# Kernel optimization log

Hardware: AMD Instinct MI355X
Metric: run time of the kernel (lower is better)

The kernel has to match this reference:

```python
import jax, jax.numpy as jnp
import numpy as np

N = 100000   # num_nodes
D = 128      # input_dim
DO = 128     # output_dim
V = 3        # num_views/relations
E = 500000   # edges per view
C = 2        # num_classes
H = D // 2   # label-attention hidden
VH = DO // 2 # view-attention hidden
EPS = 1e-5


def setup_inputs() -> dict:
    key = jax.random.key(0)
    ks = jax.random.split(key, 20)
    s = 0.05
    def nrm(k, shape):
        return jax.random.normal(k, shape, dtype=jnp.float32) * s
    return {
        'features': jax.random.normal(ks[0], (N, D), dtype=jnp.float32),
        'edge_src': jax.random.randint(ks[1], (V, E), 0, N, dtype=jnp.int32),
        'edge_dst': jax.random.randint(ks[2], (V, E), 0, N, dtype=jnp.int32),
        'edge_w': jax.random.uniform(ks[3], (V, E), dtype=jnp.float32),
        'clsW': nrm(ks[4], (D, C)), 'clsb': jnp.zeros((C,), jnp.float32),
        'attW1': nrm(ks[5], (C, D, H)), 'attb1': jnp.zeros((C, H), jnp.float32),
        'attW2': nrm(ks[6], (C, H)), 'attb2': jnp.zeros((C,), jnp.float32),
        'att_bias': jnp.float32(0.1),
        'relW': nrm(ks[7], (V, D, DO)), 'relb': jnp.zeros((V, DO), jnp.float32),
        'gateW': nrm(ks[8], (V, DO, DO)), 'gateb': jnp.zeros((V, DO), jnp.float32),
        'view_pref': jax.random.normal(ks[9], (V, DO), dtype=jnp.float32),
        'vattW1': nrm(ks[10], (DO, VH)), 'vattb1': jnp.zeros((VH,), jnp.float32),
        'vattW2': nrm(ks[11], (VH,)), 'vattb2': jnp.float32(0.0),
        'selfW': nrm(ks[12], (D, DO)), 'selfb': jnp.zeros((DO,), jnp.float32),
        'featW': nrm(ks[13], (D, DO)), 'featb': jnp.zeros((DO,), jnp.float32),
        'fusW': nrm(ks[14], (2 * DO, DO)), 'fusb': jnp.zeros((DO,), jnp.float32),
        'ln_g': jnp.ones((DO,), jnp.float32), 'ln_b': jnp.zeros((DO,), jnp.float32),
    }


def reference(features, edge_src, edge_dst, edge_w,
              clsW, clsb, attW1, attb1, attW2, attb2, att_bias,
              relW, relb, gateW, gateb,
              view_pref, vattW1, vattb1, vattW2, vattb2,
              selfW, selfb, featW, featb, fusW, fusb, ln_g, ln_b):
    # --- LabelAwareAttention ---
    class_probs = jax.nn.softmax(features @ clsW + clsb, axis=-1)          # [N,C]
    h = jax.nn.relu(jnp.einsum('nd,cdh->cnh', features, attW1) + attb1[:, None, :])
    scores = jax.nn.sigmoid(jnp.einsum('cnh,ch->cn', h, attW2) + attb2[:, None])
    node_att = jnp.sum(scores.T * class_probs, axis=-1) + att_bias         # [N]

    # --- per-view RelationAggregator (num_relations=1 -> relation weight is 1) ---
    src_f = features[edge_src]                                             # [V,E,D]
    msg = (jnp.einsum('ved,vdo->veo', src_f, relW) + relb[:, None, :]) \
          * edge_w[..., None]                                              # [V,E,DO]
    agg = jax.vmap(lambda m, d: jax.ops.segment_sum(m, d, num_segments=N))(
        msg, edge_dst)                                                     # [V,N,DO]
    gate = jax.nn.sigmoid(jnp.einsum('vno,vop->vnp', agg, gateW) + gateb[:, None, :])
    view_out = gate * agg                                                  # [V,N,DO]

    # --- ViewLevelAttention ---
    vh = jax.nn.relu(jnp.einsum('vno,oh->vnh', view_out * view_pref[:, None, :], vattW1) + vattb1)
    vscores = jnp.einsum('vnh,h->vn', vh, vattW2) + vattb2                 # [V,N]
    vweights = jax.nn.softmax(vscores, axis=0)                             # softmax over views
    combined = jnp.sum(view_out * vweights[..., None], axis=0)             # [N,DO]

    # --- fusion + residual + layer norm (dropout=0, eval) ---
    self_out = features @ selfW + selfb
    transformed = features @ featW + featb
    weighted = combined * node_att[:, None]
    fused = jax.nn.relu(jnp.concatenate([self_out, weighted], axis=-1) @ fusW + fusb)
    out = fused + transformed
    mu = jnp.mean(out, axis=-1, keepdims=True)
    var = jnp.var(out, axis=-1, keepdims=True)
    out = (out - mu) / jnp.sqrt(var + EPS) * ln_g + ln_b
    return out, class_probs
```

## Files before the change

### kernel.cpp

```cpp
#include <hip/hip_runtime.h>
#include <hip/hip_bf16.h>

#define NN 100000
#define DD 128
#define VV 3
#define EE 500000
#define TOT (VV * NN)
#define NB ((TOT + 255) / 256)
#define RGB ((NN + 127) / 128)

typedef unsigned short u16;
typedef unsigned int u32;
typedef short s8v __attribute__((ext_vector_type(8)));
typedef float f4v __attribute__((ext_vector_type(4)));

__device__ __forceinline__ float bf2f(u16 u) {
    return __uint_as_float(((u32)u) << 16);
}
__device__ __forceinline__ u16 f2bf(float f) {
    u32 x = __float_as_uint(f);
    u32 r = (x + 0x7fffu + ((x >> 16) & 1u)) >> 16;
    return (u16)r;
}

__device__ __forceinline__ void atomAddBf16x2(u16* addr, float f0, float f1) {
#if __has_builtin(__builtin_amdgcn_global_atomic_fadd_v2bf16)
    typedef short v2s __attribute__((ext_vector_type(2)));
    typedef v2s __attribute__((address_space(1)))* v2s_gp;
    v2s v;
    v.x = (short)f2bf(f0);
    v.y = (short)f2bf(f1);
    __builtin_amdgcn_global_atomic_fadd_v2bf16((v2s_gp)(void*)addr, v);
#else
    u32* p = (u32*)addr;
    u32 old = *(volatile u32*)p;
    while (true) {
        float lo = bf2f((u16)(old & 0xffffu)) + f0;
        float hi = bf2f((u16)(old >> 16)) + f1;
        u32 nv = (u32)f2bf(lo) | ((u32)f2bf(hi) << 16);
        u32 prev = atomicCAS(p, old, nv);
        if (prev == old) break;
        old = prev;
    }
#endif
}

template<int XSTR, int WSTR>
__device__ __forceinline__ void gemm16(float acc[4][4], const float* Xs,
                                       const float* Ws, int n0, int o0, int kbase) {
    #pragma unroll 4
    for (int kk = 0; kk < 64; kk += 4) {
        float4 w0 = *reinterpret_cast<const float4*>(Ws + (kk + 0) * WSTR + o0);
        float4 w1 = *reinterpret_cast<const float4*>(Ws + (kk + 1) * WSTR + o0);
        float4 w2 = *reinterpret_cast<const float4*>(Ws + (kk + 2) * WSTR + o0);
        float4 w3 = *reinterpret_cast<const float4*>(Ws + (kk + 3) * WSTR + o0);
// ... 75 lines not shown
    size_t o = ((size_t)v * 128 + n) * 128 + k;
    size_t i = ((size_t)v * 128 + k) * 128 + n;
    relWb[o]  = f2bf(relW[i]);
    gateWb[o] = f2bf(gateW[i]);
}

__global__ __launch_bounds__(128) void wprep2_kernel(
        const float* __restrict__ Wsf, const float* __restrict__ featW,
        const float* __restrict__ fusW,
        u16* __restrict__ WsfB, u16* __restrict__ featWB, u16* __restrict__ fusWbB) {
    int k = threadIdx.x;
    int n = blockIdx.x;
    WsfB[n * 128 + k]   = f2bf(Wsf[k * 128 + n]);
    featWB[n * 128 + k] = f2bf(featW[k * 128 + n]);
    fusWbB[n * 128 + k] = f2bf(fusW[(size_t)(128 + k) * 128 + n]);
}

__global__ __launch_bounds__(128) void wprep3_kernel(
        const float* __restrict__ attW1, u16* __restrict__ attW1B) {
    int k = threadIdx.x;
    int o = blockIdx.x;
    int c = o >> 6, h = o & 63;
    attW1B[o * 128 + k] = f2bf(attW1[((size_t)c * 128 + k) * 64 + h]);
}

__global__ __launch_bounds__(128) void wprep4_kernel(
        const float* __restrict__ vattW1, const float* __restrict__ view_pref,
        u16* __restrict__ vattW1p) {
    int k = threadIdx.x;
    int h = blockIdx.x & 63;
    int v = blockIdx.x >> 6;
    vattW1p[((size_t)v * 64 + h) * 128 + k] =
        f2bf(view_pref[v * 128 + k] * vattW1[k * 64 + h]);
}

__global__ __launch_bounds__(256) void featconv_kernel(
        const float* __restrict__ feat, u16* __restrict__ featB) {
    int t = blockIdx.x * 256 + threadIdx.x;
    float4 q = *reinterpret_cast<const float4*>(feat + (size_t)t * 4);
    ushort4 r;
    r.x = f2bf(q.x); r.y = f2bf(q.y); r.z = f2bf(q.z); r.w = f2bf(q.w);
    *reinterpret_cast<ushort4*>(featB + (size_t)t * 4) = r;
}


__global__ __launch_bounds__(256) void count_kernel(
        const int* __restrict__ edst, int* __restrict__ C) {
    int t = blockIdx.x * 256 + threadIdx.x;
    if (t >= VV * EE) return;
    int v = t / EE;
    atomicAdd(&C[v * NN + edst[t]], 1);
}

__global__ __launch_bounds__(256) void scanA_kernel(
        const int* __restrict__ C, int* __restrict__ bs) {
    int b = blockIdx.x, t = threadIdx.x;
    int i = b * 256 + t;
    int v = (i < TOT) ? C[i] : 0;
    __shared__ int s[256];
    s[t] = v;
    __syncthreads();
    #pragma unroll
    for (int off = 128; off > 0; off >>= 1) {
        if (t < off) s[t] += s[t + off];
        __syncthreads();
    }
// ... 297 lines not shown
    __syncthreads();
    if (tid < 64) {
        int n = tid >> 1, cc = tid & 1;
        float l = 0.f;
        for (int k = 0; k < 128; k += 4) {
            float4 x = *reinterpret_cast<const float4*>(&Xs[n][k]);
            l += x.x * clsW[(k + 0) * 2 + cc];
            l += x.y * clsW[(k + 1) * 2 + cc];
            l += x.z * clsW[(k + 2) * 2 + cc];
            l += x.w * clsW[(k + 3) * 2 + cc];
        }
        Lsc[n * 2 + cc] = l + clsb[cc];
        float s = 0.f;
        for (int u = 0; u < 16; ++u) s += red[n * 33 + cc * 16 + u];
        s += attb2[cc];
        Ssc[n * 2 + cc] = 1.f / (1.f + expf(-s));
    }
    __syncthreads();
    if (tid < 32) {
        int n = tid;
        float l0 = Lsc[n * 2], l1 = Lsc[n * 2 + 1];
        float m = fmaxf(l0, l1);
        float e0 = expf(l0 - m), e1 = expf(l1 - m);
        float inv = 1.f / (e0 + e1);
        float p0 = e0 * inv, p1 = e1 * inv;
        float na = p0 * Ssc[n * 2] + p1 * Ssc[n * 2 + 1] + att_bias[0];
        int row = row0 + n;
        node_att[row] = na;
        probs_out[row * 2]     = p0;
        probs_out[row * 2 + 1] = p1;
    }
}

__global__ __launch_bounds__(256) void relgate_mfma_kernel(
        const u16* __restrict__ relWb, const float* __restrict__ relb,
        const u16* __restrict__ gateWb, const float* __restrict__ gateb,
        const u16* __restrict__ vattW1p, const float* __restrict__ vattb1,
        const float* __restrict__ vattW2, const float* __restrict__ vattb2,
        u16* __restrict__ aggB, const float* __restrict__ wsum,
        float* __restrict__ vscores) {
    __shared__ u16 Xs[128][136];
    __shared__ u16 Wt[128][72];
    int tid = threadIdx.x;
    int wv = tid >> 6, lane = tid & 63;
    int quad = lane >> 4, l15 = lane & 15;
    int v = blockIdx.y;
    int row0 = blockIdx.x * 128;
    const size_t vbase = (size_t)v * NN;

    #pragma unroll
    for (int rep = 0; rep < 8; ++rep) {
        int flat = rep * 256 + tid;
        int n = flat >> 4, c8 = flat & 15;
        int gr = row0 + n; if (gr >= NN) gr = NN - 1;
        uint4 q = *reinterpret_cast<const uint4*>(aggB + (vbase + gr) * DD + c8 * 8);
        *reinterpret_cast<uint4*>(&Xs[n][c8 * 8]) = q;
    }

    f4v acc1[2][8], acc2[2][8];
    #pragma unroll
    for (int rt = 0; rt < 2; ++rt)
        #pragma unroll
        for (int c = 0; c < 8; ++c) {
            acc1[rt][c] = f4v{0.f, 0.f, 0.f, 0.f};
            acc2[rt][c] = f4v{0.f, 0.f, 0.f, 0.f};
        }

    const u16* W1 = relWb + (size_t)v * DD * DD;
    const u16* W2 = gateWb + (size_t)v * DD * DD;

    #pragma unroll
    for (int h = 0; h < 2; ++h) {
        #pragma unroll
        for (int rep = 0; rep < 4; ++rep) {
            int flat = rep * 256 + tid;
            int n = flat >> 3, c8 = flat & 7;
            uint4 q = *reinterpret_cast<const uint4*>(W1 + (size_t)n * DD + h * 64 + c8 * 8);
            *reinterpret_cast<uint4*>(&Wt[n][c8 * 8]) = q;
        }
        __syncthreads();
        #pragma unroll
        for (int t = 0; t < 2; ++t) {
            int kl = t * 32 + quad * 8;
            s8v a0 = *reinterpret_cast<const s8v*>(&Xs[wv * 32 + l15][h * 64 + kl]);
            s8v a1 = *reinterpret_cast<const s8v*>(&Xs[wv * 32 + 16 + l15][h * 64 + kl]);
            #pragma unroll
            for (int c = 0; c < 8; ++c) {
                s8v b = *reinterpret_cast<const s8v*>(&Wt[c * 16 + l15][kl]);
                acc1[0][c] = __builtin_amdgcn_mfma_f32_16x16x32_bf16(a0, b, acc1[0][c], 0, 0, 0);
                acc1[1][c] = __builtin_amdgcn_mfma_f32_16x16x32_bf16(a1, b, acc1[1][c], 0, 0, 0);
            }
        }
        __syncthreads();
    }

    float wsn[2][4], rb[8];
    #pragma unroll
    for (int rt = 0; rt < 2; ++rt)
        #pragma unroll
        for (int r = 0; r < 4; ++r) {
            int gr = row0 + wv * 32 + rt * 16 + quad * 4 + r;
            wsn[rt][r] = wsum[vbase + (gr < NN ? gr : NN - 1)];
        }
    #pragma unroll
    for (int c = 0; c < 8; ++c) rb[c] = relb[v * DD + c * 16 + l15];
    #pragma unroll
    for (int rt = 0; rt < 2; ++rt)
        #pragma unroll
        for (int c = 0; c < 8; ++c)
            #pragma unroll
            for (int r = 0; r < 4; ++r)
                acc1[rt][c][r] += wsn[rt][r] * rb[c];

    #pragma unroll
    for (int rt = 0; rt < 2; ++rt)
        #pragma unroll
        for (int c = 0; c < 8; ++c)
            #pragma unroll
            for (int r = 0; r < 4; ++r)
                Xs[wv * 32 + rt * 16 + quad * 4 + r][c * 16 + l15] = f2bf(acc1[rt][c][r]);
    __syncthreads();

    #pragma unroll
    for (int h = 0; h < 2; ++h) {
        #pragma unroll
        for (int rep = 0; rep < 4; ++rep) {
            int flat = rep * 256 + tid;
            int n = flat >> 3, c8 = flat & 7;
            uint4 q = *reinterpret_cast<const uint4*>(W2 + (size_t)n * DD + h * 64 + c8 * 8);
            *reinterpret_cast<uint4*>(&Wt[n][c8 * 8]) = q;
        }
        __syncthreads();
        #pragma unroll
        for (int t = 0; t < 2; ++t) {
            int kl = t * 32 + quad * 8;
            s8v a0 = *reinterpret_cast<const s8v*>(&Xs[wv * 32 + l15][h * 64 + kl]);
            s8v a1 = *reinterpret_cast<const s8v*>(&Xs[wv * 32 + 16 + l15][h * 64 + kl]);
            #pragma unroll
            for (int c = 0; c < 8; ++c) {
                s8v b = *reinterpret_cast<const s8v*>(&Wt[c * 16 + l15][kl]);
                acc2[0][c] = __builtin_amdgcn_mfma_f32_16x16x32_bf16(a0, b, acc2[0][c], 0, 0, 0);
                acc2[1][c] = __builtin_amdgcn_mfma_f32_16x16x32_bf16(a1, b, acc2[1][c], 0, 0, 0);
            }
        }
        __syncthreads();
    }

    float gb[8];
    #pragma unroll
    for (int c = 0; c < 8; ++c) gb[c] = gateb[v * DD + c * 16 + l15];
    #pragma unroll
    for (int rt = 0; rt < 2; ++rt)
        #pragma unroll
        for (int c = 0; c < 8; ++c)
            #pragma unroll
            for (int r = 0; r < 4; ++r) {
                float g = 1.f / (1.f + expf(-(acc2[rt][c][r] + gb[c])));
                Xs[wv * 32 + rt * 16 + quad * 4 + r][c * 16 + l15] = f2bf(g * acc1[rt][c][r]);
            }

    {
        const u16* Wv = vattW1p + (size_t)v * 64 * DD;
        #pragma unroll
        for (int rep = 0; rep < 4; ++rep) {
            int flat = rep * 256 + tid;
            int n = flat >> 4, c8 = flat & 15;
            uint4 q = *reinterpret_cast<const uint4*>(Wv + (size_t)n * DD + c8 * 8);
            int half = c8 >> 3;
            *reinterpret_cast<uint4*>(&Wt[half * 64 + n][(c8 & 7) * 8]) = q;
        }
    }
    __syncthreads();

    #pragma unroll
    for (int rep = 0; rep < 8; ++rep) {
        int flat = rep * 256 + tid;
        int n = flat >> 4, c8 = flat & 15;
        int gr = row0 + n;
        if (gr < NN)
            *reinterpret_cast<uint4*>(aggB + (vbase + gr) * DD + c8 * 8) =
                *reinterpret_cast<const uint4*>(&Xs[n][c8 * 8]);
    }

    f4v acc3[2][4];
    #pragma unroll
    for (int rt = 0; rt < 2; ++rt)
        #pragma unroll
        for (int c = 0; c < 4; ++c)
            acc3[rt][c] = f4v{0.f, 0.f, 0.f, 0.f};
    #pragma unroll
    for (int h = 0; h < 2; ++h) {
        #pragma unroll
        for (int t = 0; t < 2; ++t) {
            int kl = t * 32 + quad * 8;
            s8v a0 = *reinterpret_cast<const s8v*>(&Xs[wv * 32 + l15][h * 64 + kl]);
            s8v a1 = *reinterpret_cast<const s8v*>(&Xs[wv * 32 + 16 + l15][h * 64 + kl]);
            #pragma unroll
            for (int c = 0; c < 4; ++c) {
                s8v b = *reinterpret_cast<const s8v*>(&Wt[h * 64 + c * 16 + l15][kl]);
                acc3[0][c] = __builtin_amdgcn_mfma_f32_16x16x32_bf16(a0, b, acc3[0][c], 0, 0, 0);
                acc3[1][c] = __builtin_amdgcn_mfma_f32_16x16x32_bf16(a1, b, acc3[1][c], 0, 0, 0);
            }
        }
    }
    float vb1[4], vw2[4];
    #pragma unroll
    for (int c = 0; c < 4; ++c) {
        int col = c * 16 + l15;
        vb1[c] = vattb1[col];
        vw2[c] = vattW2[col];
    }
    float vb2 = vattb2[0];
    #pragma unroll
    for (int rt = 0; rt < 2; ++rt)
        #pragma unroll
        for (int r = 0; r < 4; ++r) {
            float p = 0.f;
            #pragma unroll
            for (int c = 0; c < 4; ++c) {
                float hv = acc3[rt][c][r] + vb1[c];
                hv = hv > 0.f ? hv : 0.f;
                p += hv * vw2[c];
            }
            #pragma unroll
            for (int m = 1; m < 16; m <<= 1)
                p += __shfl_xor(p, m);
            int gr = row0 + wv * 32 + rt * 16 + quad * 4 + r;
            if (l15 == 0 && gr < NN)
                vscores[vbase + gr] = p + vb2;
        }
}

__global__ __launch_bounds__(256) void relgate_kernel(
        const float* __restrict__ relW, const float* __restrict__ relb,
        const float* __restrict__ gateW, const float* __restrict__ gateb,
        u16* __restrict__ aggB, const float* __restrict__ wsum) {
    __shared__ float Xs[32][128];
// ... 110 lines not shown
    #pragma unroll
    for (int i = 0; i < 4; ++i) red[(n0 + i) * 17 + to] = part[i];
    __syncthreads();
    if (tid < 32) {
        float s = 0.f;
        for (int u = 0; u < 16; ++u) s += red[tid * 17 + u];
        vscores[(size_t)v * NN + row0 + tid] = s + vattb2[0];
    }
}

__global__ __launch_bounds__(256) void combine_kernel(
        u16* __restrict__ aggB, const float* __restrict__ vscores,
        const float* __restrict__ node_att) {
    int t = blockIdx.x * 256 + threadIdx.x;
    int n = t >> 5, c4 = t & 31;
    float s0 = vscores[n], s1 = vscores[NN + n], s2 = vscores[2 * NN + n];
    float m = fmaxf(s0, fmaxf(s1, s2));
    float e0 = expf(s0 - m), e1 = expf(s1 - m), e2 = expf(s2 - m);
    float inv = 1.f / (e0 + e1 + e2);
    float w0 = e0 * inv, w1 = e1 * inv, w2 = e2 * inv;
    float na = node_att[n];
    size_t off = (size_t)n * DD + c4 * 4;
    ushort4 q0 = *reinterpret_cast<const ushort4*>(aggB + off);
    ushort4 q1 = *reinterpret_cast<const ushort4*>(aggB + (size_t)NN * DD + off);
    ushort4 q2 = *reinterpret_cast<const ushort4*>(aggB + 2 * (size_t)NN * DD + off);
    ushort4 r;
    r.x = f2bf((bf2f(q0.x) * w0 + bf2f(q1.x) * w1 + bf2f(q2.x) * w2) * na);
    r.y = f2bf((bf2f(q0.y) * w0 + bf2f(q1.y) * w1 + bf2f(q2.y) * w2) * na);
    r.z = f2bf((bf2f(q0.z) * w0 + bf2f(q1.z) * w1 + bf2f(q2.z) * w2) * na);
    r.w = f2bf((bf2f(q0.w) * w0 + bf2f(q1.w) * w1 + bf2f(q2.w) * w2) * na);
    *reinterpret_cast<ushort4*>(aggB + off) = r;
}

__global__ __launch_bounds__(256) void final_mfma_kernel(
        const u16* __restrict__ featB, const u16* __restrict__ aggB,
        const float* __restrict__ vsc, const float* __restrict__ natt,
        const u16* __restrict__ WsfB, const u16* __restrict__ featWB,
        const u16* __restrict__ fusWbB,
        const float* __restrict__ c1, const float* __restrict__ featb,
        const float* __restrict__ ln_g, const float* __restrict__ ln_b,
        float* __restrict__ outp) {
    __shared__ u16 Xs[128][136];
    __shared__ u16 Wt[128][72];
    __shared__ float rw[3][128];
    int tid = threadIdx.x;
    int wv = tid >> 6, lane = tid & 63;
    int quad = lane >> 4, l15 = lane & 15;
    int row0 = blockIdx.x * 128;

    #pragma unroll
    for (int rep = 0; rep < 8; ++rep) {
        int flat = rep * 256 + tid;
        int n = flat >> 4, c8 = flat & 15;
        int gr = row0 + n; if (gr >= NN) gr = NN - 1;
        uint4 q = *reinterpret_cast<const uint4*>(featB + (size_t)gr * DD + c8 * 8);
        *reinterpret_cast<uint4*>(&Xs[n][c8 * 8]) = q;
    }
    if (tid < 128) {
        int gr = row0 + tid; if (gr >= NN) gr = NN - 1;
        float s0 = vsc[gr], s1 = vsc[NN + gr], s2 = vsc[2 * NN + gr];
        float m = fmaxf(s0, fmaxf(s1, s2));
        float e0 = expf(s0 - m), e1 = expf(s1 - m), e2 = expf(s2 - m);
        float inv = 1.f / (e0 + e1 + e2);
        float na = natt[gr];
        rw[0][tid] = e0 * inv * na;
        rw[1][tid] = e1 * inv * na;
        rw[2][tid] = e2 * inv * na;
    }

    f4v acc1[2][8], acc2[2][8];
    #pragma unroll
    for (int rt = 0; rt < 2; ++rt)
        #pragma unroll
        for (int c = 0; c < 8; ++c) {
            acc1[rt][c] = f4v{0.f, 0.f, 0.f, 0.f};
            acc2[rt][c] = f4v{0.f, 0.f, 0.f, 0.f};
        }

    #pragma unroll
    for (int h = 0; h < 2; ++h) {
        #pragma unroll
        for (int rep = 0; rep < 4; ++rep) {
            int flat = rep * 256 + tid;
            int n = flat >> 3, c8 = flat & 7;
            uint4 q = *reinterpret_cast<const uint4*>(WsfB + (size_t)n * DD + h * 64 + c8 * 8);
            *reinterpret_cast<uint4*>(&Wt[n][c8 * 8]) = q;
        }
        __syncthreads();
        #pragma unroll
        for (int t = 0; t < 2; ++t) {
            int kl = t * 32 + quad * 8;
            s8v a0 = *reinterpret_cast<const s8v*>(&Xs[wv * 32 + l15][h * 64 + kl]);
            s8v a1 = *reinterpret_cast<const s8v*>(&Xs[wv * 32 + 16 + l15][h * 64 + kl]);
            #pragma unroll
            for (int c = 0; c < 8; ++c) {
                s8v b = *reinterpret_cast<const s8v*>(&Wt[c * 16 + l15][kl]);
                acc1[0][c] = __builtin_amdgcn_mfma_f32_16x16x32_bf16(a0, b, acc1[0][c], 0, 0, 0);
                acc1[1][c] = __builtin_amdgcn_mfma_f32_16x16x32_bf16(a1, b, acc1[1][c], 0, 0, 0);
            }
        }
        __syncthreads();
        #pragma unroll
        for (int rep = 0; rep < 4; ++rep) {
            int flat = rep * 256 + tid;
            int n = flat >> 3, c8 = flat & 7;
            uint4 q = *reinterpret_cast<const uint4*>(featWB + (size_t)n * DD + h * 64 + c8 * 8);
            *reinterpret_cast<uint4*>(&Wt[n][c8 * 8]) = q;
        }
        __syncthreads();
        #pragma unroll
        for (int t = 0; t < 2; ++t) {
            int kl = t * 32 + quad * 8;
            s8v a0 = *reinterpret_cast<const s8v*>(&Xs[wv * 32 + l15][h * 64 + kl]);
            s8v a1 = *reinterpret_cast<const s8v*>(&Xs[wv * 32 + 16 + l15][h * 64 + kl]);
            #pragma unroll
            for (int c = 0; c < 8; ++c) {
                s8v b = *reinterpret_cast<const s8v*>(&Wt[c * 16 + l15][kl]);
                acc2[0][c] = __builtin_amdgcn_mfma_f32_16x16x32_bf16(a0, b, acc2[0][c], 0, 0, 0);
                acc2[1][c] = __builtin_amdgcn_mfma_f32_16x16x32_bf16(a1, b, acc2[1][c], 0, 0, 0);
            }
        }
        __syncthreads();
    }

    #pragma unroll
    for (int rep = 0; rep < 8; ++rep) {
        int flat = rep * 256 + tid;
        int n = flat >> 4, c8 = flat & 15;
        int gr = row0 + n; if (gr >= NN) gr = NN - 1;
        size_t off = (size_t)gr * DD + c8 * 8;
        uint4 q0 = *reinterpret_cast<const uint4*>(aggB + off);
        uint4 q1 = *reinterpret_cast<const uint4*>(aggB + (size_t)NN * DD + off);
        uint4 q2 = *reinterpret_cast<const uint4*>(aggB + 2 * (size_t)NN * DD + off);
        float w0 = rw[0][n], w1 = rw[1][n], w2 = rw[2][n];
        u32 o[4];
        const u32* a = &q0.x; const u32* b = &q1.x; const u32* c = &q2.x;
        #pragma unroll
        for (int j = 0; j < 4; ++j) {
            float lo = bf2f((u16)(a[j] & 0xffffu)) * w0 + bf2f((u16)(b[j] & 0xffffu)) * w1
                     + bf2f((u16)(c[j] & 0xffffu)) * w2;
            float hi = bf2f((u16)(a[j] >> 16)) * w0 + bf2f((u16)(b[j] >> 16)) * w1
                     + bf2f((u16)(c[j] >> 16)) * w2;
            o[j] = (u32)f2bf(lo) | ((u32)f2bf(hi) << 16);
        }
        uint4 r; r.x = o[0]; r.y = o[1]; r.z = o[2]; r.w = o[3];
        *reinterpret_cast<uint4*>(&Xs[n][c8 * 8]) = r;
    }
    #pragma unroll
    for (int h = 0; h < 2; ++h) {
        #pragma unroll
        for (int rep = 0; rep < 4; ++rep) {
            int flat = rep * 256 + tid;
            int n = flat >> 3, c8 = flat & 7;
            uint4 q = *reinterpret_cast<const uint4*>(fusWbB + (size_t)n * DD + h * 64 + c8 * 8);
            *reinterpret_cast<uint4*>(&Wt[n][c8 * 8]) = q;
        }
        __syncthreads();
        #pragma unroll
        for (int t = 0; t < 2; ++t) {
            int kl = t * 32 + quad * 8;
            s8v a0 = *reinterpret_cast<const s8v*>(&Xs[wv * 32 + l15][h * 64 + kl]);
            s8v a1 = *reinterpret_cast<const s8v*>(&Xs[wv * 32 + 16 + l15][h * 64 + kl]);
            #pragma unroll
            for (int c = 0; c < 8; ++c) {
                s8v b = *reinterpret_cast<const s8v*>(&Wt[c * 16 + l15][kl]);
                acc1[0][c] = __builtin_amdgcn_mfma_f32_16x16x32_bf16(a0, b, acc1[0][c], 0, 0, 0);
                acc1[1][c] = __builtin_amdgcn_mfma_f32_16x16x32_bf16(a1, b, acc1[1][c], 0, 0, 0);
            }
        }
        __syncthreads();
    }

    float c1j[8], fbj[8], gj[8], bj[8];
    #pragma unroll
    for (int c = 0; c < 8; ++c) {
        int col = c * 16 + l15;
        c1j[c] = c1[col];
        fbj[c] = featb[col];
        gj[c]  = ln_g[col];
        bj[c]  = ln_b[col];
    }
    #pragma unroll
    for (int rt = 0; rt < 2; ++rt)
        #pragma unroll
        for (int c = 0; c < 8; ++c)
            #pragma unroll
            for (int r = 0; r < 4; ++r) {
                float f = acc1[rt][c][r] + c1j[c];
                f = f > 0.f ? f : 0.f;
                acc1[rt][c][r] = f + acc2[rt][c][r] + fbj[c];
            }
    #pragma unroll
    for (int rt = 0; rt < 2; ++rt)
        #pragma unroll
        for (int r = 0; r < 4; ++r) {
            float s = 0.f, q = 0.f;
            #pragma unroll
            for (int c = 0; c < 8; ++c) {
                float x = acc1[rt][c][r];
                s += x; q += x * x;
            }
            #pragma unroll
            for (int m = 1; m < 16; m <<= 1) {
// ... 115 lines not shown
    const float* attb2     = (const float*)d_in[9];
    const float* att_bias  = (const float*)d_in[10];
    const float* relW      = (const float*)d_in[11];
    const float* relb      = (const float*)d_in[12];
    const float* gateW     = (const float*)d_in[13];
    const float* gateb     = (const float*)d_in[14];
    const float* view_pref = (const float*)d_in[15];
    const float* vattW1    = (const float*)d_in[16];
    const float* vattb1    = (const float*)d_in[17];
    const float* vattW2    = (const float*)d_in[18];
    const float* vattb2    = (const float*)d_in[19];
    const float* selfW     = (const float*)d_in[20];
    const float* selfb     = (const float*)d_in[21];
    const float* featW     = (const float*)d_in[22];
    const float* featb     = (const float*)d_in[23];
    const float* fusW      = (const float*)d_in[24];
    const float* fusb      = (const float*)d_in[25];
    const float* ln_g      = (const float*)d_in[26];
    const float* ln_b      = (const float*)d_in[27];

    u16*   aggB = (u16*)d_ws;
    float* wsum = (float*)(aggB + (size_t)VV * NN * DD);
    float* natt = wsum + (size_t)VV * NN;
    float* vsc  = natt + NN;
    float* Wsf  = vsc + (size_t)VV * NN;
    float* c1   = Wsf + DD * DD;
    u16* relWb  = (u16*)(c1 + DD);
    u16* gateWb = relWb + (size_t)VV * DD * DD;
    u16* WsfB   = gateWb + (size_t)VV * DD * DD;
    u16* featWB = WsfB + DD * DD;
    u16* fusWbB = featWB + DD * DD;
    u16* attW1B = fusWbB + DD * DD;
    u16* vattW1p = attW1B + DD * DD;
    int*   C    = (int*)(vattW1p + (size_t)VV * 64 * DD);
    int*   bs   = C + (size_t)TOT;
    int2*  bsw  = (int2*)(bs + NB + 1);
    u16* featB  = (u16*)(bsw + (size_t)VV * EE);
    size_t needed = (size_t)((char*)(featB + (size_t)NN * DD) - (char*)d_ws);

    float* outp  = (float*)d_out;
    float* probs = outp + (size_t)NN * DD;

    prep_kernel<<<129, 128, 0, stream>>>(selfW, selfb, fusW, fusb, Wsf, c1);
    if (ws_size >= needed) {
        featconv_kernel<<<12500, 256, 0, stream>>>(feat, featB);
        wprep_kernel<<<384, 128, 0, stream>>>(relW, gateW, relWb, gateWb);
        wprep2_kernel<<<128, 128, 0, stream>>>(Wsf, featW, fusW, WsfB, featWB, fusWbB);
        wprep3_kernel<<<128, 128, 0, stream>>>(attW1, attW1B);
        wprep4_kernel<<<192, 128, 0, stream>>>(vattW1, view_pref, vattW1p);
        label_mfma_kernel<<<RGB, 256, 0, stream>>>(featB, attW1B, clsW, clsb, attb1,
                                                   attW2, attb2, att_bias, natt, probs);
        hipMemsetAsync(C, 0, (size_t)TOT * sizeof(int), stream);
        count_kernel<<<(VV * EE + 255) / 256, 256, 0, stream>>>(edst, C);
        scanA_kernel<<<NB, 256, 0, stream>>>(C, bs);
        scanB_kernel<<<1, 1024, 0, stream>>>(bs);
        scanC_kernel<<<NB, 256, 0, stream>>>(C, bs);
        fill_kernel<<<(VV * EE + 255) / 256, 256, 0, stream>>>(esrc, edst, ew, C, bsw);
        gather_kernel<<<(VV * NN) / 4, 256, 0, stream>>>(featB, C, bsw, aggB, wsum);
        relgate_mfma_kernel<<<dim3(RGB, 3), 256, 0, stream>>>(relWb, relb, gateWb, gateb,
                                                              vattW1p, vattb1, vattW2, vattb2,
                                                              aggB, wsum, vsc);
        final_mfma_kernel<<<RGB, 256, 0, stream>>>(featB, aggB, vsc, natt,
                                                   WsfB, featWB, fusWbB,
                                                   c1, featb, ln_g, ln_b, outp);
    } else {
        label_kernel<<<3125, 256, 0, stream>>>(feat, clsW, clsb, attW1, attb1, attW2, attb2,
                                               att_bias, natt, probs);
        hipMemsetAsync(d_ws, 0,
                       (size_t)VV * NN * DD * sizeof(u16) + (size_t)VV * NN * sizeof(float),
                       stream);
        scatter_kernel<<<187500, 256, 0, stream>>>(esrc, edst, ew, feat, aggB, wsum);
        relgate_kernel<<<dim3(3125, 3), 256, 0, stream>>>(relW, relb, gateW, gateb, aggB, wsum);
        vatt_kernel<<<dim3(3125, 3), 128, 0, stream>>>(aggB, view_pref, vattW1, vattb1,
                                                       vattW2, vattb2, vsc);
        combine_kernel<<<12500, 256, 0, stream>>>(aggB, vsc, natt);
        final_kernel<<<3125, 256, 0, stream>>>(feat, aggB, Wsf, c1, fusW, featW, featb,
                                               ln_g, ln_b, outp);
    }
}
```

Baseline: 677.1 us.

## Precompose relW·gateW so rel and gate GEMMs run in parallel from registers

Adds a prep kernel that precomputes the product of relW and gateW (plus relb times gateW), so the gate pre-activation comes straight from agg and no longer waits on the rel output. This lets both GEMMs share A fragments held in registers, with fewer LDS round-trips and barriers. Final_mfma likewise loads A fragments into registers once and stages full weight tiles, and the softmax and sigmoid now use exp2/rcp intrinsics. Occupancy hints are added as launch bounds. The trade-offs are higher register pressure and a small numerical difference, since the composed weight is rounded to bf16.

```diff
diff --git a/kernel.cpp b/kernel.cpp
--- a/kernel.cpp
+++ b/kernel.cpp
@@ -21,6 +21,24 @@
     u32 x = __float_as_uint(f);
     u32 r = (x + 0x7fffu + ((x >> 16) & 1u)) >> 16;
     return (u16)r;
+}
+
+__device__ __forceinline__ float fexp2(float x) {
+#if __has_builtin(__builtin_amdgcn_exp2f)
+    return __builtin_amdgcn_exp2f(x);
+#else
+    return exp2f(x);
+#endif
+}
+__device__ __forceinline__ float frcp(float x) {
+#if __has_builtin(__builtin_amdgcn_rcpf)
+    return __builtin_amdgcn_rcpf(x);
+#else
+    return 1.f / x;
+#endif
+}
+__device__ __forceinline__ float fsigmoid(float x) {
+    return frcp(1.f + fexp2(-1.4426950408889634f * x));
 }
 
 __device__ __forceinline__ void atomAddBf16x2(u16* addr, float f0, float f1) {
@@ -162,6 +180,28 @@
     int v = blockIdx.x >> 6;
     vattW1p[((size_t)v * 64 + h) * 128 + k] =
         f2bf(view_pref[v * 128 + k] * vattW1[k * 64 + h]);
+}
+
+__global__ __launch_bounds__(128) void wprep5_kernel(
+        const float* __restrict__ relW, const float* __restrict__ gateW,
+        const float* __restrict__ relb,
+        u16* __restrict__ W12b, float* __restrict__ rgb) {
+    int p = threadIdx.x;
+    int b = blockIdx.x;
+    int v = b / 129;
+    int d = b - v * 129;
+    const float* gW = gateW + (size_t)v * 128 * 128;
+    if (d < 128) {
+        const float* rW = relW + ((size_t)v * 128 + d) * 128;
+        float acc = 0.f;
+        for (int o = 0; o < 128; ++o) acc += rW[o] * gW[o * 128 + p];
+        W12b[((size_t)v * 128 + p) * 128 + d] = f2bf(acc);
+    } else {
+        const float* rb = relb + (size_t)v * 128;
+        float acc = 0.f;
+        for (int o = 0; o < 128; ++o) acc += rb[o] * gW[o * 128 + p];
+        rgb[v * 128 + p] = acc;
+    }
 }
 
 __global__ __launch_bounds__(256) void featconv_kernel(
@@ -525,14 +565,15 @@
     }
 }
 
-__global__ __launch_bounds__(256) void relgate_mfma_kernel(
+__global__ __launch_bounds__(256, 3) void relgate_mfma_kernel(
         const u16* __restrict__ relWb, const float* __restrict__ relb,
-        const u16* __restrict__ gateWb, const float* __restrict__ gateb,
+        const u16* __restrict__ W12b, const float* __restrict__ rgb,
+        const float* __restrict__ gateb,
         const u16* __restrict__ vattW1p, const float* __restrict__ vattb1,
         const float* __restrict__ vattW2, const float* __restrict__ vattb2,
         u16* __restrict__ aggB, const float* __restrict__ wsum,
         float* __restrict__ vscores) {
-    __shared__ u16 Xs[128][136];
+    __shared__ u16 Wf[128][136];
     __shared__ u16 Wt[128][72];
     int tid = threadIdx.x;
     int wv = tid >> 6, lane = tid & 63;
@@ -547,8 +588,38 @@
         int n = flat >> 4, c8 = flat & 15;
         int gr = row0 + n; if (gr >= NN) gr = NN - 1;
         uint4 q = *reinterpret_cast<const uint4*>(aggB + (vbase + gr) * DD + c8 * 8);
-        *reinterpret_cast<uint4*>(&Xs[n][c8 * 8]) = q;
-    }
+        *reinterpret_cast<uint4*>(&Wf[n][c8 * 8]) = q;
+    }
+    __syncthreads();
+
+    s8v af[2][2][2];
+    #pragma unroll
+    for (int h = 0; h < 2; ++h)
+        #pragma unroll
+        for (int t = 0; t < 2; ++t) {
+            int kl = h * 64 + t * 32 + quad * 8;
+            af[h][t][0] = *reinterpret_cast<const s8v*>(&Wf[wv * 32 + l15][kl]);
+            af[h][t][1] = *reinterpret_cast<const s8v*>(&Wf[wv * 32 + 16 + l15][kl]);
+        }
+    __syncthreads();
+
+    const u16* W1 = relWb + (size_t)v * DD * DD;
+    const u16* W2 = W12b + (size_t)v * DD * DD;
+    #pragma unroll
+    for (int rep = 0; rep < 8; ++rep) {
+        int flat = rep * 256 + tid;
+        int n = flat >> 4, c8 = flat & 15;
+        *reinterpret_cast<uint4*>(&Wf[n][c8 * 8]) =
+            *reinterpret_cast<const uint4*>(W1 + (size_t)n * DD + c8 * 8);
+    }
+    #pragma unroll
+    for (int rep = 0; rep < 4; ++rep) {
+        int flat = rep * 256 + tid;
+        int n = flat >> 3, c8 = flat & 7;
+        *reinterpret_cast<uint4*>(&Wt[n][c8 * 8]) =
+            *reinterpret_cast<const uint4*>(W2 + (size_t)n * DD + c8 * 8);
+    }
+    __syncthreads();
 
     f4v acc1[2][8], acc2[2][8];
     #pragma unroll
@@ -559,35 +630,50 @@
             acc2[rt][c] = f4v{0.f, 0.f, 0.f, 0.f};
         }
 
-    const u16* W1 = relWb + (size_t)v * DD * DD;
-    const u16* W2 = gateWb + (size_t)v * DD * DD;
-
-    #pragma unroll
-    for (int h = 0; h < 2; ++h) {
-        #pragma unroll
-        for (int rep = 0; rep < 4; ++rep) {
-            int flat = rep * 256 + tid;
-            int n = flat >> 3, c8 = flat & 7;
-            uint4 q = *reinterpret_cast<const uint4*>(W1 + (size_t)n * DD + h * 64 + c8 * 8);
-            *reinterpret_cast<uint4*>(&Wt[n][c8 * 8]) = q;
-        }
-        __syncthreads();
+    #pragma unroll
+    for (int h = 0; h < 2; ++h)
         #pragma unroll
         for (int t = 0; t < 2; ++t) {
-            int kl = t * 32 + quad * 8;
-            s8v a0 = *reinterpret_cast<const s8v*>(&Xs[wv * 32 + l15][h * 64 + kl]);
-            s8v a1 = *reinterpret_cast<const s8v*>(&Xs[wv * 32 + 16 + l15][h * 64 + kl]);
+            int kl = h * 64 + t * 32 + quad * 8;
             #pragma unroll
             for (int c = 0; c < 8; ++c) {
-                s8v b = *reinterpret_cast<const s8v*>(&Wt[c * 16 + l15][kl]);
-                acc1[0][c] = __builtin_amdgcn_mfma_f32_16x16x32_bf16(a0, b, acc1[0][c], 0, 0, 0);
-                acc1[1][c] = __builtin_amdgcn_mfma_f32_16x16x32_bf16(a1, b, acc1[1][c], 0, 0, 0);
-            }
-        }
-        __syncthreads();
-    }
-
-    float wsn[2][4], rb[8];
+                s8v b = *reinterpret_cast<const s8v*>(&Wf[c * 16 + l15][kl]);
+                acc1[0][c] = __builtin_amdgcn_mfma_f32_16x16x32_bf16(af[h][t][0], b, acc1[0][c], 0, 0, 0);
+                acc1[1][c] = __builtin_amdgcn_mfma_f32_16x16x32_bf16(af[h][t][1], b, acc1[1][c], 0, 0, 0);
+            }
+        }
+    #pragma unroll
+    for (int t = 0; t < 2; ++t) {
+        int kl = t * 32 + quad * 8;
+        #pragma unroll
+        for (int c = 0; c < 8; ++c) {
+            s8v b = *reinterpret_cast<const s8v*>(&Wt[c * 16 + l15][kl]);
+            acc2[0][c] = __builtin_amdgcn_mfma_f32_16x16x32_bf16(af[0][t][0], b, acc2[0][c], 0, 0, 0);
+            acc2[1][c] = __builtin_amdgcn_mfma_f32_16x16x32_bf16(af[0][t][1], b, acc2[1][c], 0, 0, 0);
+        }
+    }
+    __syncthreads();
+
+    #pragma unroll
+    for (int rep = 0; rep < 4; ++rep) {
+        int flat = rep * 256 + tid;
+        int n = flat >> 3, c8 = flat & 7;
+        *reinterpret_cast<uint4*>(&Wt[n][c8 * 8]) =
+            *reinterpret_cast<const uint4*>(W2 + (size_t)n * DD + 64 + c8 * 8);
+    }
+    __syncthreads();
+    #pragma unroll
+    for (int t = 0; t < 2; ++t) {
+        int kl = t * 32 + quad * 8;
+        #pragma unroll
+        for (int c = 0; c < 8; ++c) {
+            s8v b = *reinterpret_cast<const s8v*>(&Wt[c * 16 + l15][kl]);
+            acc2[0][c] = __builtin_amdgcn_mfma_f32_16x16x32_bf16(af[1][t][0], b, acc2[0][c], 0, 0, 0);
+            acc2[1][c] = __builtin_amdgcn_mfma_f32_16x16x32_bf16(af[1][t][1], b, acc2[1][c], 0, 0, 0);
+        }
+    }
+
+    float wsn[2][4];
     #pragma unroll
     for (int rt = 0; rt < 2; ++rt)
         #pragma unroll
@@ -595,62 +681,25 @@
             int gr = row0 + wv * 32 + rt * 16 + quad * 4 + r;
             wsn[rt][r] = wsum[vbase + (gr < NN ? gr : NN - 1)];
         }
-    #pragma unroll
-    for (int c = 0; c < 8; ++c) rb[c] = relb[v * DD + c * 16 + l15];
-    #pragma unroll
-    for (int rt = 0; rt < 2; ++rt)
-        #pragma unroll
-        for (int c = 0; c < 8; ++c)
-            #pragma unroll
-            for (int r = 0; r < 4; ++r)
-                acc1[rt][c][r] += wsn[rt][r] * rb[c];
-
-    #pragma unroll
-    for (int rt = 0; rt < 2; ++rt)
-        #pragma unroll
-        for (int c = 0; c < 8; ++c)
-            #pragma unroll
-            for (int r = 0; r < 4; ++r)
-                Xs[wv * 32 + rt * 16 + quad * 4 + r][c * 16 + l15] = f2bf(acc1[rt][c][r]);
-    __syncthreads();
-
-    #pragma unroll
-    for (int h = 0; h < 2; ++h) {
-        #pragma unroll
-        for (int rep = 0; rep < 4; ++rep) {
-            int flat = rep * 256 + tid;
-            int n = flat >> 3, c8 = flat & 7;
-            uint4 q = *reinterpret_cast<const uint4*>(W2 + (size_t)n * DD + h * 64 + c8 * 8);
-            *reinterpret_cast<uint4*>(&Wt[n][c8 * 8]) = q;
-        }
-        __syncthreads();
-        #pragma unroll
-        for (int t = 0; t < 2; ++t) {
-            int kl = t * 32 + quad * 8;
-            s8v a0 = *reinterpret_cast<const s8v*>(&Xs[wv * 32 + l15][h * 64 + kl]);
-            s8v a1 = *reinterpret_cast<const s8v*>(&Xs[wv * 32 + 16 + l15][h * 64 + kl]);
-            #pragma unroll
-            for (int c = 0; c < 8; ++c) {
-                s8v b = *reinterpret_cast<const s8v*>(&Wt[c * 16 + l15][kl]);
-                acc2[0][c] = __builtin_amdgcn_mfma_f32_16x16x32_bf16(a0, b, acc2[0][c], 0, 0, 0);
-                acc2[1][c] = __builtin_amdgcn_mfma_f32_16x16x32_bf16(a1, b, acc2[1][c], 0, 0, 0);
-            }
-        }
-        __syncthreads();
-    }
-
-    float gb[8];
-    #pragma unroll
-    for (int c = 0; c < 8; ++c) gb[c] = gateb[v * DD + c * 16 + l15];
+    float rb[8], rg2[8], gb[8];
+    #pragma unroll
+    for (int c = 0; c < 8; ++c) {
+        int col = c * 16 + l15;
+        rb[c]  = relb[v * DD + col];
+        rg2[c] = rgb[v * DD + col];
+        gb[c]  = gateb[v * DD + col];
+    }
     #pragma unroll
     for (int rt = 0; rt < 2; ++rt)
         #pragma unroll
         for (int c = 0; c < 8; ++c)
             #pragma unroll
             for (int r = 0; r < 4; ++r) {
-                float g = 1.f / (1.f + expf(-(acc2[rt][c][r] + gb[c])));
-                Xs[wv * 32 + rt * 16 + quad * 4 + r][c * 16 + l15] = f2bf(g * acc1[rt][c][r]);
-            }
+                float a = acc1[rt][c][r] + wsn[rt][r] * rb[c];
+                float g = fsigmoid(acc2[rt][c][r] + wsn[rt][r] * rg2[c] + gb[c]);
+                Wf[wv * 32 + rt * 16 + quad * 4 + r][c * 16 + l15] = f2bf(g * a);
+            }
+    __syncthreads();
 
     {
         const u16* Wv = vattW1p + (size_t)v * 64 * DD;
@@ -663,8 +712,15 @@
             *reinterpret_cast<uint4*>(&Wt[half * 64 + n][(c8 & 7) * 8]) = q;
         }
     }
-    __syncthreads();
-
+    s8v a2[2][2][2];
+    #pragma unroll
+    for (int h = 0; h < 2; ++h)
+        #pragma unroll
+        for (int t = 0; t < 2; ++t) {
+            int kl = h * 64 + t * 32 + quad * 8;
+            a2[h][t][0] = *reinterpret_cast<const s8v*>(&Wf[wv * 32 + l15][kl]);
+            a2[h][t][1] = *reinterpret_cast<const s8v*>(&Wf[wv * 32 + 16 + l15][kl]);
+        }
     #pragma unroll
     for (int rep = 0; rep < 8; ++rep) {
         int flat = rep * 256 + tid;
@@ -672,8 +728,9 @@
         int gr = row0 + n;
         if (gr < NN)
             *reinterpret_cast<uint4*>(aggB + (vbase + gr) * DD + c8 * 8) =
-                *reinterpret_cast<const uint4*>(&Xs[n][c8 * 8]);
-    }
+                *reinterpret_cast<const uint4*>(&Wf[n][c8 * 8]);
+    }
+    __syncthreads();
 
     f4v acc3[2][4];
     #pragma unroll
@@ -682,20 +739,17 @@
         for (int c = 0; c < 4; ++c)
             acc3[rt][c] = f4v{0.f, 0.f, 0.f, 0.f};
     #pragma unroll
-    for (int h = 0; h < 2; ++h) {
+    for (int h = 0; h < 2; ++h)
         #pragma unroll
         for (int t = 0; t < 2; ++t) {
             int kl = t * 32 + quad * 8;
-            s8v a0 = *reinterpret_cast<const s8v*>(&Xs[wv * 32 + l15][h * 64 + kl]);
-            s8v a1 = *reinterpret_cast<const s8v*>(&Xs[wv * 32 + 16 + l15][h * 64 + kl]);
             #pragma unroll
             for (int c = 0; c < 4; ++c) {
                 s8v b = *reinterpret_cast<const s8v*>(&Wt[h * 64 + c * 16 + l15][kl]);
-                acc3[0][c] = __builtin_amdgcn_mfma_f32_16x16x32_bf16(a0, b, acc3[0][c], 0, 0, 0);
-                acc3[1][c] = __builtin_amdgcn_mfma_f32_16x16x32_bf16(a1, b, acc3[1][c], 0, 0, 0);
-            }
-        }
-    }
+                acc3[0][c] = __builtin_amdgcn_mfma_f32_16x16x32_bf16(a2[h][t][0], b, acc3[0][c], 0, 0, 0);
+                acc3[1][c] = __builtin_amdgcn_mfma_f32_16x16x32_bf16(a2[h][t][1], b, acc3[1][c], 0, 0, 0);
+            }
+        }
     float vb1[4], vw2[4];
     #pragma unroll
     for (int c = 0; c < 4; ++c) {
@@ -872,7 +926,7 @@
     *reinterpret_cast<ushort4*>(aggB + off) = r;
 }
 
-__global__ __launch_bounds__(256) void final_mfma_kernel(
+__global__ __launch_bounds__(256, 3) void final_mfma_kernel(
         const u16* __restrict__ featB, const u16* __restrict__ aggB,
         const float* __restrict__ vsc, const float* __restrict__ natt,
         const u16* __restrict__ WsfB, const u16* __restrict__ featWB,
@@ -880,9 +934,8 @@
         const float* __restrict__ c1, const float* __restrict__ featb,
         const float* __restrict__ ln_g, const float* __restrict__ ln_b,
         float* __restrict__ outp) {
-    __shared__ u16 Xs[128][136];
+    __shared__ u16 Wf[128][136];
     __shared__ u16 Wt[128][72];
-    __shared__ float rw[3][128];
     int tid = threadIdx.x;
     int wv = tid >> 6, lane = tid & 63;
     int quad = lane >> 4, l15 = lane & 15;
@@ -894,19 +947,50 @@
         int n = flat >> 4, c8 = flat & 15;
         int gr = row0 + n; if (gr >= NN) gr = NN - 1;
         uint4 q = *reinterpret_cast<const uint4*>(featB + (size_t)gr * DD + c8 * 8);
-        *reinterpret_cast<uint4*>(&Xs[n][c8 * 8]) = q;
+        *reinterpret_cast<uint4*>(&Wf[n][c8 * 8]) = q;
     }
     if (tid < 128) {
         int gr = row0 + tid; if (gr >= NN) gr = NN - 1;
         float s0 = vsc[gr], s1 = vsc[NN + gr], s2 = vsc[2 * NN + gr];
         float m = fmaxf(s0, fmaxf(s1, s2));
-        float e0 = expf(s0 - m), e1 = expf(s1 - m), e2 = expf(s2 - m);
-        float inv = 1.f / (e0 + e1 + e2);
-        float na = natt[gr];
-        rw[0][tid] = e0 * inv * na;
-        rw[1][tid] = e1 * inv * na;
-        rw[2][tid] = e2 * inv * na;
-    }
+        const float L2E = 1.4426950408889634f;
+        float e0 = fexp2((s0 - m) * L2E);
+        float e1 = fexp2((s1 - m) * L2E);
+        float e2 = fexp2((s2 - m) * L2E);
+        float na = natt[gr] * frcp(e0 + e1 + e2);
+        float* rwp = reinterpret_cast<float*>(&Wf[tid][128]);
+        rwp[0] = e0 * na;
+        rwp[1] = e1 * na;
+        rwp[2] = e2 * na;
+    }
+    __syncthreads();
+
+    s8v af[2][2][2];
+    #pragma unroll
+    for (int h = 0; h < 2; ++h)
+        #pragma unroll
+        for (int t = 0; t < 2; ++t) {
+            int kl = h * 64 + t * 32 + quad * 8;
+            af[h][t][0] = *reinterpret_cast<const s8v*>(&Wf[wv * 32 + l15][kl]);
+            af[h][t][1] = *reinterpret_cast<const s8v*>(&Wf[wv * 32 + 16 + l15][kl]);
+        }
+    __syncthreads();
+
+    #pragma unroll
+    for (int rep = 0; rep < 8; ++rep) {
+        int flat = rep * 256 + tid;
+        int n = flat >> 4, c8 = flat & 15;
+        *reinterpret_cast<uint4*>(&Wf[n][c8 * 8]) =
+            *reinterpret_cast<const uint4*>(WsfB + (size_t)n * DD + c8 * 8);
+    }
+    #pragma unroll
+    for (int rep = 0; rep < 4; ++rep) {
+        int flat = rep * 256 + tid;
+        int n = flat >> 3, c8 = flat & 7;
+        *reinterpret_cast<uint4*>(&Wt[n][c8 * 8]) =
+            *reinterpret_cast<const uint4*>(featWB + (size_t)n * DD + c8 * 8);
+    }
+    __syncthreads();
 
     f4v acc1[2][8], acc2[2][8];
     #pragma unroll
@@ -918,49 +1002,45 @@
         }
 
     #pragma unroll
-    for (int h = 0; h < 2; ++h) {
-        #pragma unroll
-        for (int rep = 0; rep < 4; ++rep) {
-            int flat = rep * 256 + tid;
-            int n = flat >> 3, c8 = flat & 7;
-            uint4 q = *reinterpret_cast<const uint4*>(WsfB + (size_t)n * DD + h * 64 + c8 * 8);
-            *reinterpret_cast<uint4*>(&Wt[n][c8 * 8]) = q;
-        }
-        __syncthreads();
+    for (int h = 0; h < 2; ++h)
         #pragma unroll
         for (int t = 0; t < 2; ++t) {
-            int kl = t * 32 + quad * 8;
-            s8v a0 = *reinterpret_cast<const s8v*>(&Xs[wv * 32 + l15][h * 64 + kl]);
-            s8v a1 = *reinterpret_cast<const s8v*>(&Xs[wv * 32 + 16 + l15][h * 64 + kl]);
+            int kl = h * 64 + t * 32 + quad * 8;
             #pragma unroll
             for (int c = 0; c < 8; ++c) {
-                s8v b = *reinterpret_cast<const s8v*>(&Wt[c * 16 + l15][kl]);
-                acc1[0][c] = __builtin_amdgcn_mfma_f32_16x16x32_bf16(a0, b, acc1[0][c], 0, 0, 0);
-                acc1[1][c] = __builtin_amdgcn_mfma_f32_16x16x32_bf16(a1, b, acc1[1][c], 0, 0, 0);
-            }
-        }
-        __syncthreads();
-        #pragma unroll
-        for (int rep = 0; rep < 4; ++rep) {
-            int flat = rep * 256 + tid;
-            int n = flat >> 3, c8 = flat & 7;
-            uint4 q = *reinterpret_cast<const uint4*>(featWB + (size_t)n * DD + h * 64 + c8 * 8);
-            *reinterpret_cast<uint4*>(&Wt[n][c8 * 8]) = q;
-        }
-        __syncthreads();
-        #pragma unroll
-        for (int t = 0; t < 2; ++t) {
-            int kl = t * 32 + quad * 8;
-            s8v a0 = *reinterpret_cast<const s8v*>(&Xs[wv * 32 + l15][h * 64 + kl]);
-            s8v a1 = *reinterpret_cast<const s8v*>(&Xs[wv * 32 + 16 + l15][h * 64 + kl]);
-            #pragma unroll
-            for (int c = 0; c < 8; ++c) {
-                s8v b = *reinterpret_cast<const s8v*>(&Wt[c * 16 + l15][kl]);
-                acc2[0][c] = __builtin_amdgcn_mfma_f32_16x16x32_bf16(a0, b, acc2[0][c], 0, 0, 0);
-                acc2[1][c] = __builtin_amdgcn_mfma_f32_16x16x32_bf16(a1, b, acc2[1][c], 0, 0, 0);
-            }
-        }
-        __syncthreads();
+                s8v b = *reinterpret_cast<const s8v*>(&Wf[c * 16 + l15][kl]);
+                acc1[0][c] = __builtin_amdgcn_mfma_f32_16x16x32_bf16(af[h][t][0], b, acc1[0][c], 0, 0, 0);
+                acc1[1][c] = __builtin_amdgcn_mfma_f32_16x16x32_bf16(af[h][t][1], b, acc1[1][c], 0, 0, 0);
+            }
+        }
+    #pragma unroll
+    for (int t = 0; t < 2; ++t) {
+        int kl = t * 32 + quad * 8;
+        #pragma unroll
+        for (int c = 0; c < 8; ++c) {
+            s8v b = *reinterpret_cast<const s8v*>(&Wt[c * 16 + l15][kl]);
+            acc2[0][c] = __builtin_amdgcn_mfma_f32_16x16x32_bf16(af[0][t][0], b, acc2[0][c], 0, 0, 0);
+            acc2[1][c] = __builtin_amdgcn_mfma_f32_16x16x32_bf16(af[0][t][1], b, acc2[1][c], 0, 0, 0);
+        }
+    }
+    __syncthreads();
+    #pragma unroll
+    for (int rep = 0; rep < 4; ++rep) {
+        int flat = rep * 256 + tid;
+        int n = flat >> 3, c8 = flat & 7;
+        *reinterpret_cast<uint4*>(&Wt[n][c8 * 8]) =
+            *reinterpret_cast<const uint4*>(featWB + (size_t)n * DD + 64 + c8 * 8);
+    }
+    __syncthreads();
+    #pragma unroll
+    for (int t = 0; t < 2; ++t) {
+        int kl = t * 32 + quad * 8;
+        #pragma unroll
+        for (int c = 0; c < 8; ++c) {
+            s8v b = *reinterpret_cast<const s8v*>(&Wt[c * 16 + l15][kl]);
+            acc2[0][c] = __builtin_amdgcn_mfma_f32_16x16x32_bf16(af[1][t][0], b, acc2[0][c], 0, 0, 0);
+            acc2[1][c] = __builtin_amdgcn_mfma_f32_16x16x32_bf16(af[1][t][1], b, acc2[1][c], 0, 0, 0);
+        }
     }
 
     #pragma unroll
@@ -972,7 +1052,8 @@
         uint4 q0 = *reinterpret_cast<const uint4*>(aggB + off);
         uint4 q1 = *reinterpret_cast<const uint4*>(aggB + (size_t)NN * DD + off);
         uint4 q2 = *reinterpret_cast<const uint4*>(aggB + 2 * (size_t)NN * DD + off);
-        float w0 = rw[0][n], w1 = rw[1][n], w2 = rw[2][n];
+        const float* rwp = reinterpret_cast<const float*>(&Wf[n][128]);
+        float w0 = rwp[0], w1 = rwp[1], w2 = rwp[2];
         u32 o[4];
         const u32* a = &q0.x; const u32* b = &q1.x; const u32* c = &q2.x;
         #pragma unroll
@@ -984,31 +1065,50 @@
             o[j] = (u32)f2bf(lo) | ((u32)f2bf(hi) << 16);
         }
         uint4 r; r.x = o[0]; r.y = o[1]; r.z = o[2]; r.w = o[3];
-        *reinterpret_cast<uint4*>(&Xs[n][c8 * 8]) = r;
-    }
-    #pragma unroll
-    for (int h = 0; h < 2; ++h) {
-        #pragma unroll
-        for (int rep = 0; rep < 4; ++rep) {
-            int flat = rep * 256 + tid;
-            int n = flat >> 3, c8 = flat & 7;
-            uint4 q = *reinterpret_cast<const uint4*>(fusWbB + (size_t)n * DD + h * 64 + c8 * 8);
-            *reinterpret_cast<uint4*>(&Wt[n][c8 * 8]) = q;
-        }
-        __syncthreads();
-        #pragma unroll
-        for (int t = 0; t < 2; ++t) {
-            int kl = t * 32 + quad * 8;
-            s8v a0 = *reinterpret_cast<const s8v*>(&Xs[wv * 32 + l15][h * 64 + kl]);
-            s8v a1 = *reinterpret_cast<const s8v*>(&Xs[wv * 32 + 16 + l15][h * 64 + kl]);
-            #pragma unroll
-            for (int c = 0; c < 8; ++c) {
-                s8v b = *reinterpret_cast<const s8v*>(&Wt[c * 16 + l15][kl]);
-                acc1[0][c] = __builtin_amdgcn_mfma_f32_16x16x32_bf16(a0, b, acc1[0][c], 0, 0, 0);
-                acc1[1][c] = __builtin_amdgcn_mfma_f32_16x16x32_bf16(a1, b, acc1[1][c], 0, 0, 0);
-            }
-        }
-        __syncthreads();
+        *reinterpret_cast<uint4*>(&Wf[n][c8 * 8]) = r;
+    }
+    __syncthreads();
+
+    #pragma unroll
+    for (int rep = 0; rep < 4; ++rep) {
+        int flat = rep * 256 + tid;
+        int n = flat >> 3, c8 = flat & 7;
+        *reinterpret_cast<uint4*>(&Wt[n][c8 * 8]) =
+            *reinterpret_cast<const uint4*>(fusWbB + (size_t)n * DD + c8 * 8);
+    }
+    __syncthreads();
+    #pragma unroll
+    for (int t = 0; t < 2; ++t) {
+        int kl = t * 32 + quad * 8;
+        s8v a0 = *reinterpret_cast<const s8v*>(&Wf[wv * 32 + l15][kl]);
+        s8v a1 = *reinterpret_cast<const s8v*>(&Wf[wv * 32 + 16 + l15][kl]);
+        #pragma unroll
+        for (int c = 0; c < 8; ++c) {
+            s8v b = *reinterpret_cast<const s8v*>(&Wt[c * 16 + l15][kl]);
+            acc1[0][c] = __builtin_amdgcn_mfma_f32_16x16x32_bf16(a0, b, acc1[0][c], 0, 0, 0);
+            acc1[1][c] = __builtin_amdgcn_mfma_f32_16x16x32_bf16(a1, b, acc1[1][c], 0, 0, 0);
+        }
+    }
+    __syncthreads();
+    #pragma unroll
+    for (int rep = 0; rep < 4; ++rep) {
+        int flat = rep * 256 + tid;
+        int n = flat >> 3, c8 = flat & 7;
+        *reinterpret_cast<uint4*>(&Wt[n][c8 * 8]) =
+            *reinterpret_cast<const uint4*>(fusWbB + (size_t)n * DD + 64 + c8 * 8);
+    }
+    __syncthreads();
+    #pragma unroll
+    for (int t = 0; t < 2; ++t) {
+        int kl = t * 32 + quad * 8;
+        s8v a0 = *reinterpret_cast<const s8v*>(&Wf[wv * 32 + l15][64 + kl]);
+        s8v a1 = *reinterpret_cast<const s8v*>(&Wf[wv * 32 + 16 + l15][64 + kl]);
+        #pragma unroll
+        for (int c = 0; c < 8; ++c) {
+            s8v b = *reinterpret_cast<const s8v*>(&Wt[c * 16 + l15][kl]);
+            acc1[0][c] = __builtin_amdgcn_mfma_f32_16x16x32_bf16(a0, b, acc1[0][c], 0, 0, 0);
+            acc1[1][c] = __builtin_amdgcn_mfma_f32_16x16x32_bf16(a1, b, acc1[1][c], 0, 0, 0);
+        }
     }
 
     float c1j[8], fbj[8], gj[8], bj[8];
@@ -1190,7 +1290,9 @@
     u16* fusWbB = featWB + DD * DD;
     u16* attW1B = fusWbB + DD * DD;
     u16* vattW1p = attW1B + DD * DD;
-    int*   C    = (int*)(vattW1p + (size_t)VV * 64 * DD);
+    u16* W12b   = vattW1p + (size_t)VV * 64 * DD;
+    float* rgb  = (float*)(W12b + (size_t)VV * DD * DD);
+    int*   C    = (int*)(rgb + VV * DD);
     int*   bs   = C + (size_t)TOT;
     int2*  bsw  = (int2*)(bs + NB + 1);
     u16* featB  = (u16*)(bsw + (size_t)VV * EE);
@@ -1206,6 +1308,7 @@
         wprep2_kernel<<<128, 128, 0, stream>>>(Wsf, featW, fusW, WsfB, featWB, fusWbB);
         wprep3_kernel<<<128, 128, 0, stream>>>(attW1, attW1B);
         wprep4_kernel<<<192, 128, 0, stream>>>(vattW1, view_pref, vattW1p);
+        wprep5_kernel<<<VV * 129, 128, 0, stream>>>(relW, gateW, relb, W12b, rgb);
         label_mfma_kernel<<<RGB, 256, 0, stream>>>(featB, attW1B, clsW, clsb, attb1,
                                                    attW2, attb2, att_bias, natt, probs);
         hipMemsetAsync(C, 0, (size_t)TOT * sizeof(int), stream);
@@ -1215,7 +1318,7 @@
         scanC_kernel<<<NB, 256, 0, stream>>>(C, bs);
         fill_kernel<<<(VV * EE + 255) / 256, 256, 0, stream>>>(esrc, edst, ew, C, bsw);
         gather_kernel<<<(VV * NN) / 4, 256, 0, stream>>>(featB, C, bsw, aggB, wsum);
-        relgate_mfma_kernel<<<dim3(RGB, 3), 256, 0, stream>>>(relWb, relb, gateWb, gateb,
+        relgate_mfma_kernel<<<dim3(RGB, 3), 256, 0, stream>>>(relWb, relb, W12b, rgb, gateb,
                                                               vattW1p, vattb1, vattW2, vattb2,
                                                               aggB, wsum, vsc);
         final_mfma_kernel<<<RGB, 256, 0, stream>>>(featB, aggB, vsc, natt,
```

New measurement: 661.3 us. 1.02x faster.
